# Optimization experiments

Hardware: AMD Instinct MI355X
Metric: run time of the kernel (lower is better)

Reference implementation:

```python
import jax, jax.numpy as jnp
import numpy as np

NEG_MIN = jnp.finfo(jnp.float32).min


def setup_inputs() -> dict:
    key = jax.random.key(0)
    kq, kk, kv, km = jax.random.split(key, 4)
    B, H, S, D = 2, 16, 2048, 64
    return {
        "query": jax.random.normal(kq, (B, H, S, D), dtype=jnp.float32),
        "key": jax.random.normal(kk, (B, H, S, D), dtype=jnp.float32),
        "value": jax.random.normal(kv, (B, H, S, D), dtype=jnp.float32),
        "attention_mask": jax.random.randint(km, (B, S), 0, 2, dtype=jnp.int32),
    }


def reference(query, key, value, attention_mask):
    # query/key/value: [B, H, S, D]; attention_mask: [B, S] (1 = keep, 0 = pad)
    D = query.shape[-1]
    scores = jnp.einsum("bhqd,bhkd->bhqk", query, key) / jnp.sqrt(jnp.float32(D))
    # 2-D mask branch: (1 - mask) * finfo.min added as additive bias
    pad = (1.0 - attention_mask.astype(jnp.float32))[:, None, None, :] * NEG_MIN
    scores = scores + pad
    # softmax in fp32 (scale_attention_softmax_in_fp32=True), cast back to query dtype
    probs = jax.nn.softmax(scores.astype(jnp.float32), axis=-1).astype(query.dtype)
    # attention_dropout = 0.0 -> no dropout
    out = jnp.einsum("bhqk,bhkd->bhqd", probs, value)
    return out
```

## Files before the change

kernel.cpp:

```cpp
#include <hip/hip_runtime.h>

typedef __attribute__((ext_vector_type(8))) short short8;
typedef __attribute__((ext_vector_type(16))) float f32x16;
typedef __attribute__((ext_vector_type(4))) int int4v;

#define LOG2E 1.4426950408889634f

#if __has_builtin(__builtin_amdgcn_exp2f)
#define EXP2(x) __builtin_amdgcn_exp2f(x)
#else
#define EXP2(x) exp2f(x)
#endif

__device__ __forceinline__ unsigned cvtpk(float lo, float hi) {
    unsigned r;
    asm("v_cvt_pk_bf16_f32 %0, %1, %2" : "=v"(r) : "v"(lo), "v"(hi));
    return r;
}

__global__ __launch_bounds__(256) void attn_fwd(
    const float* __restrict__ Q, const float* __restrict__ K,
    const float* __restrict__ V, const int* __restrict__ M,
    float* __restrict__ O)
{
    constexpr int S = 2048, D = 64, KVB = 64, NT = S / KVB;
    __shared__ unsigned short k_lds[2][KVB * D];
    __shared__ unsigned short vt_lds[2][D * KVB];
    __shared__ float bias_lds[S];
    __shared__ float l_buf[4][32];

    const int t = threadIdx.x;
    const int lane = t & 63, wid = t >> 6;
    const int l31 = lane & 31, hi = lane >> 5;

    const int lin = blockIdx.x;
    const int wgid = (lin & 7) * 64 + (lin >> 3);
    const int bh = wgid >> 4;
    const int qblk = wgid & 15;
    const int b = bh >> 4;

    const int* mrow = M + b * S;
    for (int i = t; i < S; i += 256)
        bias_lds[i] = mrow[i] ? -24.0f : -__builtin_inff();

    const int qrow0 = qblk * 128 + wid * 32;
    const float* qp = Q + ((size_t)bh * S + qrow0 + l31) * D;
    const float qs = 0.125f * LOG2E;
    short8 qf[4];
    #pragma unroll
    for (int c = 0; c < 4; ++c) {
        const float* p = qp + c * 16 + hi * 8;
        float4 x = *(const float4*)p;
        float4 y = *(const float4*)(p + 4);
        int4v w = { (int)cvtpk(x.x * qs, x.y * qs), (int)cvtpk(x.z * qs, x.w * qs),
                    (int)cvtpk(y.x * qs, y.y * qs), (int)cvtpk(y.z * qs, y.w * qs) };
        qf[c] = __builtin_bit_cast(short8, w);
    }

    f32x16 acc0 = {0,0,0,0,0,0,0,0,0,0,0,0,0,0,0,0};
    f32x16 acc1 = {0,0,0,0,0,0,0,0,0,0,0,0,0,0,0,0};
    float l = 0.0f;

    const int skey = t >> 2, sds2 = (t & 3) * 32;
    const int swzk = (skey & 7) << 4;
    const int kwb = skey * 128;
    const int vkey2 = lane * 2;
    const int vds = wid * 16;

    const int krow0 = l31 * 128;
    const int krow1 = (32 + l31) * 128;
    const int kx = (hi * 16) ^ ((l31 & 7) << 4);
    const int vrow0 = l31 * 128;
    const int vrow1 = (32 + l31) * 128;

    const float* kpt = K + (size_t)bh * S * D + (size_t)skey * D + (t & 3) * 16;
    const float* vpt = V + (size_t)bh * S * D + (size_t)lane * D + vds;

    float4 ka0, ka1, ka2, ka3, vb0, vb1, vb2, vb3;

    auto load_tile = [&]() {
        ka0 = ((const float4*)kpt)[0]; ka1 = ((const float4*)kpt)[1];
        ka2 = ((const float4*)kpt)[2]; ka3 = ((const float4*)kpt)[3];
        vb0 = ((const float4*)vpt)[0]; vb1 = ((const float4*)vpt)[1];
        vb2 = ((const float4*)vpt)[2]; vb3 = ((const float4*)vpt)[3];
        kpt += KVB * D; vpt += KVB * D;
    };
    auto write_tile = [&](unsigned short* kdst, unsigned short* vdst) {
        int4v w0 = { (int)cvtpk(ka0.x,ka0.y), (int)cvtpk(ka0.z,ka0.w),
                     (int)cvtpk(ka1.x,ka1.y), (int)cvtpk(ka1.z,ka1.w) };
        int4v w1 = { (int)cvtpk(ka2.x,ka2.y), (int)cvtpk(ka2.z,ka2.w),
                     (int)cvtpk(ka3.x,ka3.y), (int)cvtpk(ka3.z,ka3.w) };
        *(int4v*)((char*)kdst + kwb + (sds2 ^ swzk)) = w0;
        *(int4v*)((char*)kdst + kwb + ((sds2 + 16) ^ swzk)) = w1;
        unsigned cc[8] = { cvtpk(vb0.x,vb0.y), cvtpk(vb0.z,vb0.w),
                           cvtpk(vb1.x,vb1.y), cvtpk(vb1.z,vb1.w),
                           cvtpk(vb2.x,vb2.y), cvtpk(vb2.z,vb2.w),
                           cvtpk(vb3.x,vb3.y), cvtpk(vb3.z,vb3.w) };
        #pragma unroll
        for (int i = 0; i < 16; ++i) {
            int row = vds + i;
            int off = row * 128 + (vkey2 ^ ((row & 7) << 4));
            unsigned val = (i & 1) ? (cc[i >> 1] >> 16) : (cc[i >> 1] & 0xffffu);
            *(unsigned short*)((char*)vdst + off) = (unsigned short)val;
        }
    };

    load_tile();
    write_tile(k_lds[0], vt_lds[0]);
    __syncthreads();

    #pragma unroll 2
    for (int it = 0; it < NT; ++it) {
        const int cur = it & 1;
        const bool more = (it + 1 < NT);
        if (more) load_tile();

        const char* kc = (const char*)k_lds[cur];
        const char* vc = (const char*)vt_lds[cur];
        const int ktoff = it * KVB;

        f32x16 s0 = {0,0,0,0,0,0,0,0,0,0,0,0,0,0,0,0};
        f32x16 s1 = {0,0,0,0,0,0,0,0,0,0,0,0,0,0,0,0};
        __builtin_amdgcn_s_setprio(1);
        #pragma unroll
        for (int c = 0; c < 4; ++c) {
            short8 kaf = *(const short8*)(kc + krow0 + (kx ^ (c << 5)));
            short8 kbf = *(const short8*)(kc + krow1 + (kx ^ (c << 5)));
            s0 = __builtin_amdgcn_mfma_f32_32x32x16_bf16(kaf, qf[c], s0, 0, 0, 0);
            s1 = __builtin_amdgcn_mfma_f32_32x32x16_bf16(kbf, qf[c], s1, 0, 0, 0);
        }
        __builtin_amdgcn_s_setprio(0);

        float rsp0 = 0.0f, rsp1 = 0.0f, rsp2 = 0.0f, rsp3 = 0.0f;
        #pragma unroll
        for (int rg = 0; rg < 4; ++rg) {
            float4 bz0 = *(const float4*)&bias_lds[ktoff + rg * 8 + hi * 4];
            float4 bz1 = *(const float4*)&bias_lds[ktoff + 32 + rg * 8 + hi * 4];
            const float* z0 = (const float*)&bz0;
            const float* z1 = (const float*)&bz1;
            float rp = 0.0f;
            #pragma unroll
            for (int j = 0; j < 4; ++j) {
                int r = rg * 4 + j;
                float e0 = EXP2(s0[r] + z0[j]);
                float e1 = EXP2(s1[r] + z1[j]);
                s0[r] = e0; s1[r] = e1;
                rp += e0 + e1;
            }
            if (rg == 0) rsp0 = rp; else if (rg == 1) rsp1 = rp;
            else if (rg == 2) rsp2 = rp; else rsp3 = rp;
        }
        float rs = (rsp0 + rsp1) + (rsp2 + rsp3);
        rs += __shfl_xor(rs, 32);
        l += rs;

        short8 pw[4];
        #pragma unroll
        for (int w = 0; w < 4; ++w) {
            int r0 = (w & 1) * 8;
            float q0 = (w >> 1) ? s1[r0+0] : s0[r0+0];
            float q1 = (w >> 1) ? s1[r0+1] : s0[r0+1];
            float q2 = (w >> 1) ? s1[r0+2] : s0[r0+2];
            float q3 = (w >> 1) ? s1[r0+3] : s0[r0+3];
            float q4 = (w >> 1) ? s1[r0+4] : s0[r0+4];
            float q5 = (w >> 1) ? s1[r0+5] : s0[r0+5];
            float q6 = (w >> 1) ? s1[r0+6] : s0[r0+6];
            float q7 = (w >> 1) ? s1[r0+7] : s0[r0+7];
            unsigned x0 = cvtpk(q0, q1);
            unsigned x1 = cvtpk(q2, q3);
            unsigned x2 = cvtpk(q4, q5);
            unsigned x3 = cvtpk(q6, q7);
            unsigned sx0 = (unsigned)__shfl_xor((int)x0, 32);
            unsigned sx1 = (unsigned)__shfl_xor((int)x1, 32);
            unsigned sx2 = (unsigned)__shfl_xor((int)x2, 32);
            unsigned sx3 = (unsigned)__shfl_xor((int)x3, 32);
            int4v wv = { (int)(hi ? sx2 : x0),
                         (int)(hi ? sx3 : x1),
                         (int)(hi ? x2 : sx0),
                         (int)(hi ? x3 : sx1) };
            pw[w] = __builtin_bit_cast(short8, wv);
        }

        __builtin_amdgcn_s_setprio(1);
        #pragma unroll
        for (int w = 0; w < 4; ++w) {
            short8 vf0 = *(const short8*)(vc + vrow0 + (kx ^ (w << 5)));
            short8 vf1 = *(const short8*)(vc + vrow1 + (kx ^ (w << 5)));
            acc0 = __builtin_amdgcn_mfma_f32_32x32x16_bf16(pw[w], vf0, acc0, 0, 0, 0);
            acc1 = __builtin_amdgcn_mfma_f32_32x32x16_bf16(pw[w], vf1, acc1, 0, 0, 0);
        }
        __builtin_amdgcn_s_setprio(0);

        if (more) write_tile(k_lds[cur ^ 1], vt_lds[cur ^ 1]);
        __syncthreads();
    }

    if (hi == 0) l_buf[wid][l31] = 1.0f / l;
    __syncthreads();

    float* ob = O + ((size_t)bh * S + qrow0) * D;
    #pragma unroll
    for (int rg = 0; rg < 4; ++rg) {
        float4 invl = *(const float4*)&l_buf[wid][rg * 8 + hi * 4];
        const float* iv = (const float*)&invl;
        #pragma unroll
        for (int j = 0; j < 4; ++j) {
            int r = rg * 4 + j;
            int qr = rg * 8 + hi * 4 + j;
            ob[qr * 64 + l31] = acc0[r] * iv[j];
            ob[qr * 64 + 32 + l31] = acc1[r] * iv[j];
        }
    }
}

extern "C" void kernel_launch(void* const* d_in, const int* in_sizes, int n_in,
                              void* d_out, int out_size, void* d_ws, size_t ws_size,
                              hipStream_t stream) {
    const float* Q = (const float*)d_in[0];
    const float* K = (const float*)d_in[1];
    const float* V = (const float*)d_in[2];
    const int*   M = (const int*)d_in[3];
    float* O = (float*)d_out;
    attn_fwd<<<dim3(512), dim3(256), 0, stream>>>(Q, K, V, M, O);
}
```

Before: 153.1 us.

## Split KV sequence across two workgroups and add combine kernel

Splits the key/value sequence into two halves so 1024 workgroups each process half the keys, writing unnormalized partial outputs and row sums to workspace. A second kernel sums the two partials and normalizes. This targets low occupancy, since 512 workgroups may underfill the GPU's compute units. In exchange it adds a workspace round-trip of partial outputs and an extra launch. It also simplifies the V-transpose swizzle to use i&7, which matches row&7 because vds is a multiple of 16.

```diff
diff --git a/kernel.cpp b/kernel.cpp
--- a/kernel.cpp
+++ b/kernel.cpp
@@ -18,29 +18,31 @@
     return r;
 }
 
-__global__ __launch_bounds__(256) void attn_fwd(
+__global__ __launch_bounds__(256, 4) void attn_fwd_split(
     const float* __restrict__ Q, const float* __restrict__ K,
     const float* __restrict__ V, const int* __restrict__ M,
-    float* __restrict__ O)
+    float* __restrict__ Opart, float* __restrict__ lpart)
 {
-    constexpr int S = 2048, D = 64, KVB = 64, NT = S / KVB;
+    constexpr int S = 2048, D = 64, KVB = 64, SPLIT = 1024, NT = SPLIT / KVB;
     __shared__ unsigned short k_lds[2][KVB * D];
     __shared__ unsigned short vt_lds[2][D * KVB];
-    __shared__ float bias_lds[S];
-    __shared__ float l_buf[4][32];
+    __shared__ float bias_lds[SPLIT];
+    __shared__ float pad_[16];
 
     const int t = threadIdx.x;
     const int lane = t & 63, wid = t >> 6;
     const int l31 = lane & 31, hi = lane >> 5;
 
     const int lin = blockIdx.x;
-    const int wgid = (lin & 7) * 64 + (lin >> 3);
-    const int bh = wgid >> 4;
+    const int wgid = (lin & 7) * 128 + (lin >> 3);
+    const int split = wgid >> 9;
+    const int bh = (wgid >> 4) & 31;
     const int qblk = wgid & 15;
     const int b = bh >> 4;
-
-    const int* mrow = M + b * S;
-    for (int i = t; i < S; i += 256)
+    const int soff = split * SPLIT;
+
+    const int* mrow = M + b * S + soff;
+    for (int i = t; i < SPLIT; i += 256)
         bias_lds[i] = mrow[i] ? -24.0f : -__builtin_inff();
 
     const int qrow0 = qblk * 128 + wid * 32;
@@ -73,8 +75,8 @@
     const int vrow0 = l31 * 128;
     const int vrow1 = (32 + l31) * 128;
 
-    const float* kpt = K + (size_t)bh * S * D + (size_t)skey * D + (t & 3) * 16;
-    const float* vpt = V + (size_t)bh * S * D + (size_t)lane * D + vds;
+    const float* kpt = K + (size_t)bh * S * D + (size_t)(soff + skey) * D + (t & 3) * 16;
+    const float* vpt = V + (size_t)bh * S * D + (size_t)(soff + lane) * D + vds;
 
     float4 ka0, ka1, ka2, ka3, vb0, vb1, vb2, vb3;
 
@@ -99,7 +101,7 @@
         #pragma unroll
         for (int i = 0; i < 16; ++i) {
             int row = vds + i;
-            int off = row * 128 + (vkey2 ^ ((row & 7) << 4));
+            int off = row * 128 + (vkey2 ^ ((i & 7) << 4));
             unsigned val = (i & 1) ? (cc[i >> 1] >> 16) : (cc[i >> 1] & 0xffffu);
             *(unsigned short*)((char*)vdst + off) = (unsigned short)val;
         }
@@ -195,6 +197,215 @@
         __syncthreads();
     }
 
+    float* ob = Opart + ((size_t)split * 32 * S + (size_t)bh * S + qrow0) * D;
+    #pragma unroll
+    for (int rg = 0; rg < 4; ++rg) {
+        #pragma unroll
+        for (int j = 0; j < 4; ++j) {
+            int r = rg * 4 + j;
+            int qr = rg * 8 + hi * 4 + j;
+            ob[qr * 64 + l31] = acc0[r];
+            ob[qr * 64 + 32 + l31] = acc1[r];
+        }
+    }
+    if (hi == 0)
+        lpart[split * 65536 + bh * 2048 + qrow0 + l31] = l;
+    (void)pad_;
+}
+
+__global__ __launch_bounds__(256) void attn_combine(
+    const float* __restrict__ Opart, const float* __restrict__ lpart,
+    float* __restrict__ O)
+{
+    const int idx4 = blockIdx.x * 256 + threadIdx.x;
+    const int row = idx4 >> 4;
+    const float4* A0 = (const float4*)Opart;
+    const float4* A1 = A0 + 1048576;
+    float inv = 1.0f / (lpart[row] + lpart[65536 + row]);
+    float4 a = A0[idx4], b = A1[idx4];
+    float4 o;
+    o.x = (a.x + b.x) * inv; o.y = (a.y + b.y) * inv;
+    o.z = (a.z + b.z) * inv; o.w = (a.w + b.w) * inv;
+    ((float4*)O)[idx4] = o;
+}
+
+__global__ __launch_bounds__(256) void attn_fwd(
+    const float* __restrict__ Q, const float* __restrict__ K,
+    const float* __restrict__ V, const int* __restrict__ M,
+    float* __restrict__ O)
+{
+    constexpr int S = 2048, D = 64, KVB = 64, NT = S / KVB;
+    __shared__ unsigned short k_lds[2][KVB * D];
+    __shared__ unsigned short vt_lds[2][D * KVB];
+    __shared__ float bias_lds[S];
+    __shared__ float l_buf[4][32];
+
+    const int t = threadIdx.x;
+    const int lane = t & 63, wid = t >> 6;
+    const int l31 = lane & 31, hi = lane >> 5;
+
+    const int lin = blockIdx.x;
+    const int wgid = (lin & 7) * 64 + (lin >> 3);
+    const int bh = wgid >> 4;
+    const int qblk = wgid & 15;
+    const int b = bh >> 4;
+
+    const int* mrow = M + b * S;
+    for (int i = t; i < S; i += 256)
+        bias_lds[i] = mrow[i] ? -24.0f : -__builtin_inff();
+
+    const int qrow0 = qblk * 128 + wid * 32;
+    const float* qp = Q + ((size_t)bh * S + qrow0 + l31) * D;
+    const float qs = 0.125f * LOG2E;
+    short8 qf[4];
+    #pragma unroll
+    for (int c = 0; c < 4; ++c) {
+        const float* p = qp + c * 16 + hi * 8;
+        float4 x = *(const float4*)p;
+        float4 y = *(const float4*)(p + 4);
+        int4v w = { (int)cvtpk(x.x * qs, x.y * qs), (int)cvtpk(x.z * qs, x.w * qs),
+                    (int)cvtpk(y.x * qs, y.y * qs), (int)cvtpk(y.z * qs, y.w * qs) };
+        qf[c] = __builtin_bit_cast(short8, w);
+    }
+
+    f32x16 acc0 = {0,0,0,0,0,0,0,0,0,0,0,0,0,0,0,0};
+    f32x16 acc1 = {0,0,0,0,0,0,0,0,0,0,0,0,0,0,0,0};
+    float l = 0.0f;
+
+    const int skey = t >> 2, sds2 = (t & 3) * 32;
+    const int swzk = (skey & 7) << 4;
+    const int kwb = skey * 128;
+    const int vkey2 = lane * 2;
+    const int vds = wid * 16;
+
+    const int krow0 = l31 * 128;
+    const int krow1 = (32 + l31) * 128;
+    const int kx = (hi * 16) ^ ((l31 & 7) << 4);
+    const int vrow0 = l31 * 128;
+    const int vrow1 = (32 + l31) * 128;
+
+    const float* kpt = K + (size_t)bh * S * D + (size_t)skey * D + (t & 3) * 16;
+    const float* vpt = V + (size_t)bh * S * D + (size_t)lane * D + vds;
+
+    float4 ka0, ka1, ka2, ka3, vb0, vb1, vb2, vb3;
+
+    auto load_tile = [&]() {
+        ka0 = ((const float4*)kpt)[0]; ka1 = ((const float4*)kpt)[1];
+        ka2 = ((const float4*)kpt)[2]; ka3 = ((const float4*)kpt)[3];
+        vb0 = ((const float4*)vpt)[0]; vb1 = ((const float4*)vpt)[1];
+        vb2 = ((const float4*)vpt)[2]; vb3 = ((const float4*)vpt)[3];
+        kpt += KVB * D; vpt += KVB * D;
+    };
+    auto write_tile = [&](unsigned short* kdst, unsigned short* vdst) {
+        int4v w0 = { (int)cvtpk(ka0.x,ka0.y), (int)cvtpk(ka0.z,ka0.w),
+                     (int)cvtpk(ka1.x,ka1.y), (int)cvtpk(ka1.z,ka1.w) };
+        int4v w1 = { (int)cvtpk(ka2.x,ka2.y), (int)cvtpk(ka2.z,ka2.w),
+                     (int)cvtpk(ka3.x,ka3.y), (int)cvtpk(ka3.z,ka3.w) };
+        *(int4v*)((char*)kdst + kwb + (sds2 ^ swzk)) = w0;
+        *(int4v*)((char*)kdst + kwb + ((sds2 + 16) ^ swzk)) = w1;
+        unsigned cc[8] = { cvtpk(vb0.x,vb0.y), cvtpk(vb0.z,vb0.w),
+                           cvtpk(vb1.x,vb1.y), cvtpk(vb1.z,vb1.w),
+                           cvtpk(vb2.x,vb2.y), cvtpk(vb2.z,vb2.w),
+                           cvtpk(vb3.x,vb3.y), cvtpk(vb3.z,vb3.w) };
+        #pragma unroll
+        for (int i = 0; i < 16; ++i) {
+            int row = vds + i;
+            int off = row * 128 + (vkey2 ^ ((i & 7) << 4));
+            unsigned val = (i & 1) ? (cc[i >> 1] >> 16) : (cc[i >> 1] & 0xffffu);
+            *(unsigned short*)((char*)vdst + off) = (unsigned short)val;
+        }
+    };
+
+    load_tile();
+    write_tile(k_lds[0], vt_lds[0]);
+    __syncthreads();
+
+    #pragma unroll 2
+    for (int it = 0; it < NT; ++it) {
+        const int cur = it & 1;
+        const bool more = (it + 1 < NT);
+        if (more) load_tile();
+
+        const char* kc = (const char*)k_lds[cur];
+        const char* vc = (const char*)vt_lds[cur];
+        const int ktoff = it * KVB;
+
+        f32x16 s0 = {0,0,0,0,0,0,0,0,0,0,0,0,0,0,0,0};
+        f32x16 s1 = {0,0,0,0,0,0,0,0,0,0,0,0,0,0,0,0};
+        __builtin_amdgcn_s_setprio(1);
+        #pragma unroll
+        for (int c = 0; c < 4; ++c) {
+            short8 kaf = *(const short8*)(kc + krow0 + (kx ^ (c << 5)));
+            short8 kbf = *(const short8*)(kc + krow1 + (kx ^ (c << 5)));
+            s0 = __builtin_amdgcn_mfma_f32_32x32x16_bf16(kaf, qf[c], s0, 0, 0, 0);
+            s1 = __builtin_amdgcn_mfma_f32_32x32x16_bf16(kbf, qf[c], s1, 0, 0, 0);
+        }
+        __builtin_amdgcn_s_setprio(0);
+
+        float rsp0 = 0.0f, rsp1 = 0.0f, rsp2 = 0.0f, rsp3 = 0.0f;
+        #pragma unroll
+        for (int rg = 0; rg < 4; ++rg) {
+            float4 bz0 = *(const float4*)&bias_lds[ktoff + rg * 8 + hi * 4];
+            float4 bz1 = *(const float4*)&bias_lds[ktoff + 32 + rg * 8 + hi * 4];
+            const float* z0 = (const float*)&bz0;
+            const float* z1 = (const float*)&bz1;
+            float rp = 0.0f;
+            #pragma unroll
+            for (int j = 0; j < 4; ++j) {
+                int r = rg * 4 + j;
+                float e0 = EXP2(s0[r] + z0[j]);
+                float e1 = EXP2(s1[r] + z1[j]);
+                s0[r] = e0; s1[r] = e1;
+                rp += e0 + e1;
+            }
+            if (rg == 0) rsp0 = rp; else if (rg == 1) rsp1 = rp;
+            else if (rg == 2) rsp2 = rp; else rsp3 = rp;
+        }
+        float rs = (rsp0 + rsp1) + (rsp2 + rsp3);
+        rs += __shfl_xor(rs, 32);
+        l += rs;
+
+        short8 pw[4];
+        #pragma unroll
+        for (int w = 0; w < 4; ++w) {
+            int r0 = (w & 1) * 8;
+            float q0 = (w >> 1) ? s1[r0+0] : s0[r0+0];
+            float q1 = (w >> 1) ? s1[r0+1] : s0[r0+1];
+            float q2 = (w >> 1) ? s1[r0+2] : s0[r0+2];
+            float q3 = (w >> 1) ? s1[r0+3] : s0[r0+3];
+            float q4 = (w >> 1) ? s1[r0+4] : s0[r0+4];
+            float q5 = (w >> 1) ? s1[r0+5] : s0[r0+5];
+            float q6 = (w >> 1) ? s1[r0+6] : s0[r0+6];
+            float q7 = (w >> 1) ? s1[r0+7] : s0[r0+7];
+            unsigned x0 = cvtpk(q0, q1);
+            unsigned x1 = cvtpk(q2, q3);
+            unsigned x2 = cvtpk(q4, q5);
+            unsigned x3 = cvtpk(q6, q7);
+            unsigned sx0 = (unsigned)__shfl_xor((int)x0, 32);
+            unsigned sx1 = (unsigned)__shfl_xor((int)x1, 32);
+            unsigned sx2 = (unsigned)__shfl_xor((int)x2, 32);
+            unsigned sx3 = (unsigned)__shfl_xor((int)x3, 32);
+            int4v wv = { (int)(hi ? sx2 : x0),
+                         (int)(hi ? sx3 : x1),
+                         (int)(hi ? x2 : sx0),
+                         (int)(hi ? x3 : sx1) };
+            pw[w] = __builtin_bit_cast(short8, wv);
+        }
+
+        __builtin_amdgcn_s_setprio(1);
+        #pragma unroll
+        for (int w = 0; w < 4; ++w) {
+            short8 vf0 = *(const short8*)(vc + vrow0 + (kx ^ (w << 5)));
+            short8 vf1 = *(const short8*)(vc + vrow1 + (kx ^ (w << 5)));
+            acc0 = __builtin_amdgcn_mfma_f32_32x32x16_bf16(pw[w], vf0, acc0, 0, 0, 0);
+            acc1 = __builtin_amdgcn_mfma_f32_32x32x16_bf16(pw[w], vf1, acc1, 0, 0, 0);
+        }
+        __builtin_amdgcn_s_setprio(0);
+
+        if (more) write_tile(k_lds[cur ^ 1], vt_lds[cur ^ 1]);
+        __syncthreads();
+    }
+
     if (hi == 0) l_buf[wid][l31] = 1.0f / l;
     __syncthreads();
 
@@ -221,5 +432,14 @@
     const float* V = (const float*)d_in[2];
     const int*   M = (const int*)d_in[3];
     float* O = (float*)d_out;
-    attn_fwd<<<dim3(512), dim3(256), 0, stream>>>(Q, K, V, M, O);
+
+    const size_t need = (size_t)2 * 32 * 2048 * 64 * 4 + (size_t)2 * 65536 * 4;
+    if (ws_size >= need) {
+        float* Opart = (float*)d_ws;
+        float* lpart = Opart + (size_t)2 * 32 * 2048 * 64;
+        attn_fwd_split<<<dim3(1024), dim3(256), 0, stream>>>(Q, K, V, M, Opart, lpart);
+        attn_combine<<<dim3(4096), dim3(256), 0, stream>>>(Opart, lpart, O);
+    } else {
+        attn_fwd<<<dim3(512), dim3(256), 0, stream>>>(Q, K, V, M, O);
+    }
 }
```

Result: slower. 209.4 us (+36.8%).

## Split KV sequence across two wave groups per block and merge partial outputs

Applied to the files above, without the earlier changes.

Doubles the block to 512 threads. Two groups of four waves each process half of the key/value sequence for the same 128 query rows, each with its own double-buffered LDS tiles. At the end, the second group writes its unnormalized accumulators and row sums to shared memory, and the first group adds them and normalizes. This is meant to raise the number of waves per CU and halve each wave's serial KV loop, since the grid has only 512 blocks. The cost is a larger LDS footprint per block and an extra shared-memory reduction step. Merging partials without a running max is only valid because the kernel uses a fixed exponent offset.

```diff
diff --git a/kernel.cpp b/kernel.cpp
--- a/kernel.cpp
+++ b/kernel.cpp
@@ -18,20 +18,25 @@
     return r;
 }
 
-__global__ __launch_bounds__(256) void attn_fwd(
+__global__ __launch_bounds__(512, 4) void attn_fwd8(
     const float* __restrict__ Q, const float* __restrict__ K,
     const float* __restrict__ V, const int* __restrict__ M,
     float* __restrict__ O)
 {
-    constexpr int S = 2048, D = 64, KVB = 64, NT = S / KVB;
-    __shared__ unsigned short k_lds[2][KVB * D];
-    __shared__ unsigned short vt_lds[2][D * KVB];
+    constexpr int S = 2048, D = 64, KVB = 64, NT = 16;
+    __shared__ __align__(16) char smem[65536];
     __shared__ float bias_lds[S];
-    __shared__ float l_buf[4][32];
+    __shared__ float l_buf[8][32];
+
+    unsigned short* kreg = (unsigned short*)smem;
+    unsigned short* vreg = (unsigned short*)(smem + 32768);
+    float* obuf = (float*)smem;
 
     const int t = threadIdx.x;
     const int lane = t & 63, wid = t >> 6;
     const int l31 = lane & 31, hi = lane >> 5;
+    const int h = wid >> 2, qw = wid & 3;
+    const int t255 = t & 255;
 
     const int lin = blockIdx.x;
     const int wgid = (lin & 7) * 64 + (lin >> 3);
@@ -40,10 +45,10 @@
     const int b = bh >> 4;
 
     const int* mrow = M + b * S;
-    for (int i = t; i < S; i += 256)
+    for (int i = t; i < S; i += 512)
         bias_lds[i] = mrow[i] ? -24.0f : -__builtin_inff();
 
-    const int qrow0 = qblk * 128 + wid * 32;
+    const int qrow0 = qblk * 128 + qw * 32;
     const float* qp = Q + ((size_t)bh * S + qrow0 + l31) * D;
     const float qs = 0.125f * LOG2E;
     short8 qf[4];
@@ -61,11 +66,11 @@
     f32x16 acc1 = {0,0,0,0,0,0,0,0,0,0,0,0,0,0,0,0};
     float l = 0.0f;
 
-    const int skey = t >> 2, sds2 = (t & 3) * 32;
+    const int skey = t255 >> 2, sds2 = (t255 & 3) * 32;
     const int swzk = (skey & 7) << 4;
     const int kwb = skey * 128;
     const int vkey2 = lane * 2;
-    const int vds = wid * 16;
+    const int vds = qw * 16;
 
     const int krow0 = l31 * 128;
     const int krow1 = (32 + l31) * 128;
@@ -73,8 +78,9 @@
     const int vrow0 = l31 * 128;
     const int vrow1 = (32 + l31) * 128;
 
-    const float* kpt = K + (size_t)bh * S * D + (size_t)skey * D + (t & 3) * 16;
-    const float* vpt = V + (size_t)bh * S * D + (size_t)lane * D + vds;
+    const int soff = h * 1024;
+    const float* kpt = K + (size_t)bh * S * D + (size_t)(soff + skey) * D + (t255 & 3) * 16;
+    const float* vpt = V + (size_t)bh * S * D + (size_t)(soff + lane) * D + vds;
 
     float4 ka0, ka1, ka2, ka3, vb0, vb1, vb2, vb3;
 
@@ -85,13 +91,15 @@
         vb2 = ((const float4*)vpt)[2]; vb3 = ((const float4*)vpt)[3];
         kpt += KVB * D; vpt += KVB * D;
     };
-    auto write_tile = [&](unsigned short* kdst, unsigned short* vdst) {
+    auto write_tile = [&](int c) {
+        char* kdst = (char*)kreg + (h * 2 + c) * 8192;
+        char* vdst = (char*)vreg + (h * 2 + c) * 8192;
         int4v w0 = { (int)cvtpk(ka0.x,ka0.y), (int)cvtpk(ka0.z,ka0.w),
                      (int)cvtpk(ka1.x,ka1.y), (int)cvtpk(ka1.z,ka1.w) };
         int4v w1 = { (int)cvtpk(ka2.x,ka2.y), (int)cvtpk(ka2.z,ka2.w),
                      (int)cvtpk(ka3.x,ka3.y), (int)cvtpk(ka3.z,ka3.w) };
-        *(int4v*)((char*)kdst + kwb + (sds2 ^ swzk)) = w0;
-        *(int4v*)((char*)kdst + kwb + ((sds2 + 16) ^ swzk)) = w1;
+        *(int4v*)(kdst + kwb + (sds2 ^ swzk)) = w0;
+        *(int4v*)(kdst + kwb + ((sds2 + 16) ^ swzk)) = w1;
         unsigned cc[8] = { cvtpk(vb0.x,vb0.y), cvtpk(vb0.z,vb0.w),
                            cvtpk(vb1.x,vb1.y), cvtpk(vb1.z,vb1.w),
                            cvtpk(vb2.x,vb2.y), cvtpk(vb2.z,vb2.w),
@@ -99,14 +107,14 @@
         #pragma unroll
         for (int i = 0; i < 16; ++i) {
             int row = vds + i;
-            int off = row * 128 + (vkey2 ^ ((row & 7) << 4));
+            int off = row * 128 + (vkey2 ^ ((i & 7) << 4));
             unsigned val = (i & 1) ? (cc[i >> 1] >> 16) : (cc[i >> 1] & 0xffffu);
-            *(unsigned short*)((char*)vdst + off) = (unsigned short)val;
+            *(unsigned short*)(vdst + off) = (unsigned short)val;
         }
     };
 
     load_tile();
-    write_tile(k_lds[0], vt_lds[0]);
+    write_tile(0);
     __syncthreads();
 
     #pragma unroll 2
@@ -115,9 +123,9 @@
         const bool more = (it + 1 < NT);
         if (more) load_tile();
 
-        const char* kc = (const char*)k_lds[cur];
-        const char* vc = (const char*)vt_lds[cur];
-        const int ktoff = it * KVB;
+        const char* kc = (const char*)kreg + (h * 2 + cur) * 8192;
+        const char* vc = (const char*)vreg + (h * 2 + cur) * 8192;
+        const int ktoff = soff + it * KVB;
 
         f32x16 s0 = {0,0,0,0,0,0,0,0,0,0,0,0,0,0,0,0};
         f32x16 s1 = {0,0,0,0,0,0,0,0,0,0,0,0,0,0,0,0};
@@ -191,24 +199,42 @@
         }
         __builtin_amdgcn_s_setprio(0);
 
-        if (more) write_tile(k_lds[cur ^ 1], vt_lds[cur ^ 1]);
+        if (more) write_tile(cur ^ 1);
         __syncthreads();
     }
 
-    if (hi == 0) l_buf[wid][l31] = 1.0f / l;
+    if (hi == 0) l_buf[wid][l31] = l;
+    if (h == 1) {
+        #pragma unroll
+        for (int rg = 0; rg < 4; ++rg) {
+            #pragma unroll
+            for (int j = 0; j < 4; ++j) {
+                int r = rg * 4 + j;
+                int qr = rg * 8 + hi * 4 + j;
+                obuf[(qw * 32 + qr) * 64 + l31] = acc0[r];
+                obuf[(qw * 32 + qr) * 64 + 32 + l31] = acc1[r];
+            }
+        }
+    }
     __syncthreads();
-
-    float* ob = O + ((size_t)bh * S + qrow0) * D;
-    #pragma unroll
-    for (int rg = 0; rg < 4; ++rg) {
-        float4 invl = *(const float4*)&l_buf[wid][rg * 8 + hi * 4];
-        const float* iv = (const float*)&invl;
-        #pragma unroll
-        for (int j = 0; j < 4; ++j) {
-            int r = rg * 4 + j;
-            int qr = rg * 8 + hi * 4 + j;
-            ob[qr * 64 + l31] = acc0[r] * iv[j];
-            ob[qr * 64 + 32 + l31] = acc1[r] * iv[j];
+    if (h == 0) {
+        float* ob = O + ((size_t)bh * S + qrow0) * D;
+        #pragma unroll
+        for (int rg = 0; rg < 4; ++rg) {
+            float4 la = *(const float4*)&l_buf[qw][rg * 8 + hi * 4];
+            float4 lb = *(const float4*)&l_buf[qw + 4][rg * 8 + hi * 4];
+            const float* pa = (const float*)&la;
+            const float* pb = (const float*)&lb;
+            #pragma unroll
+            for (int j = 0; j < 4; ++j) {
+                int r = rg * 4 + j;
+                int qr = rg * 8 + hi * 4 + j;
+                float inv = 1.0f / (pa[j] + pb[j]);
+                float o0 = acc0[r] + obuf[(qw * 32 + qr) * 64 + l31];
+                float o1 = acc1[r] + obuf[(qw * 32 + qr) * 64 + 32 + l31];
+                ob[qr * 64 + l31] = o0 * inv;
+                ob[qr * 64 + 32 + l31] = o1 * inv;
+            }
         }
     }
 }
@@ -221,5 +247,5 @@
     const float* V = (const float*)d_in[2];
     const int*   M = (const int*)d_in[3];
     float* O = (float*)d_out;
-    attn_fwd<<<dim3(512), dim3(256), 0, stream>>>(Q, K, V, M, O);
+    attn_fwd8<<<dim3(512), dim3(512), 0, stream>>>(Q, K, V, M, O);
 }
```

Result: slower. 207.0 us (+35.3%).
